# Kernel optimization log

Hardware: AMD Instinct MI355X
Metric: run time of the kernel (lower is better)

The kernel has to match this reference:

```python
import jax, jax.numpy as jnp
import numpy as np

H, KD, VD = 12, 64, 64  # num_heads, k_dim, v_dim
EPS = 1e-12

def _l2norm(x, axis):
    n = jnp.linalg.norm(x, axis=axis, keepdims=True)
    return x / jnp.maximum(n, EPS)

def setup_inputs() -> dict:
    key = jax.random.key(0)
    ks = jax.random.split(key, 6)
    d1, d2 = 768, 768
    return {
        "x1": jax.random.normal(ks[0], (2048, d1), jnp.float32),
        "x2": jax.random.normal(ks[1], (8192, d2), jnp.float32),
        "Wq": jax.random.normal(ks[2], (H * KD, d1), jnp.float32) * 0.03,
        "Wk": jax.random.normal(ks[3], (H * KD, d2), jnp.float32) * 0.03,
        "Wv": jax.random.normal(ks[4], (H * VD, d2), jnp.float32) * 0.03,
        "Wo": jax.random.normal(ks[5], (d1, H * VD), jnp.float32) * 0.03,
        "invt": 20,
    }

def reference(x1, x2, Wq, Wk, Wv, Wo, invt):
    B1 = x1.shape[0]
    B2 = x2.shape[0]
    # Linear (no bias): y = x @ W.T, then split heads
    q = (x1 @ Wq.T).reshape(B1, H, KD)  # [B1,H,KD]
    k = (x2 @ Wk.T).reshape(B2, H, KD)  # [B2,H,KD]
    v = (x2 @ Wv.T).reshape(B2, H, VD)  # [B2,H,VD]
    # per-head L2 normalization over feature dim (cosine attention)
    q = _l2norm(q, axis=-1)
    k = _l2norm(k, axis=-1)
    attn = jnp.einsum("bhd,nhd->hbn", q, k) * jnp.float32(invt)  # [H,B1,B2]
    attn = jax.nn.softmax(attn, axis=-1)
    out = jnp.einsum("hbn,nhd->bhd", attn, v).reshape(B1, H * VD)
    out = out @ Wo.T  # [B1, in_dim1]
    return _l2norm(out, axis=1)
```

## Files before the change

### kernel.cpp

```cpp
#include <hip/hip_runtime.h>
#include <hip/hip_bf16.h>
#include <math.h>

#define B1 2048
#define B2 8192
#define NH 12
#define DH 64
#define DMODEL 768

typedef __attribute__((ext_vector_type(8))) short short8;
typedef __attribute__((ext_vector_type(4))) float floatx4;
typedef __attribute__((ext_vector_type(8))) unsigned short ushort8;
typedef __attribute__((ext_vector_type(4))) unsigned short ushort4v;

static __device__ __forceinline__ unsigned short f2bf(float f) {
  __bf16 b = (__bf16)f;
  return __builtin_bit_cast(unsigned short, b);
}

template <bool L2N, bool F32OUT>
static __device__ __forceinline__ void gemm_tile_f32(
    const float* __restrict__ Ag, const float* __restrict__ Bg,
    void* __restrict__ Cv, int M, int N, int K, int m0, int n0,
    unsigned short* sA, unsigned short* sB) {
  const int tid = threadIdx.x;
  const int wave = tid >> 6;
  const int lane = tid & 63;
  const int wm = wave >> 1;
  const int wn = wave & 1;
  const int n15 = lane & 15;
  const int quad = lane >> 4;
  const int srow = lane >> 2;
  const int cpl = (lane & 3) ^ (srow >> 2);
  const int nstep = K >> 5;

  floatx4 acc[4][4];
#pragma unroll
  for (int i = 0; i < 4; ++i)
#pragma unroll
    for (int j = 0; j < 4; ++j) acc[i][j] = (floatx4){0.f, 0.f, 0.f, 0.f};

  float4 ar[2][2], br[2][2];
#pragma unroll
  for (int jj = 0; jj < 2; ++jj) {
    const int row = (wave * 2 + jj) * 16 + srow;
    const size_t ga = (size_t)(m0 + row) * K + cpl * 8;
    const size_t gb = (size_t)(n0 + row) * K + cpl * 8;
    ar[jj][0] = *(const float4*)&Ag[ga];
    ar[jj][1] = *(const float4*)&Ag[ga + 4];
    br[jj][0] = *(const float4*)&Bg[gb];
    br[jj][1] = *(const float4*)&Bg[gb + 4];
  }
#pragma unroll
  for (int jj = 0; jj < 2; ++jj) {
    const int j = wave * 2 + jj;
    const float4 a0 = ar[jj][0], a1 = ar[jj][1];
    const float4 b0 = br[jj][0], b1 = br[jj][1];
    ushort8 ah = {f2bf(a0.x), f2bf(a0.y), f2bf(a0.z), f2bf(a0.w),
                  f2bf(a1.x), f2bf(a1.y), f2bf(a1.z), f2bf(a1.w)};
    ushort8 bh = {f2bf(b0.x), f2bf(b0.y), f2bf(b0.z), f2bf(b0.w),
                  f2bf(b1.x), f2bf(b1.y), f2bf(b1.z), f2bf(b1.w)};
    *(ushort8*)&sA[j * 512 + lane * 8] = ah;
    *(ushort8*)&sB[j * 512 + lane * 8] = bh;
  }
  if (nstep > 1) {
#pragma unroll
    for (int jj = 0; jj < 2; ++jj) {
      const int row = (wave * 2 + jj) * 16 + srow;
      const size_t ga = (size_t)(m0 + row) * K + 32 + cpl * 8;
      const size_t gb = (size_t)(n0 + row) * K + 32 + cpl * 8;
      ar[jj][0] = *(const float4*)&Ag[ga];
      ar[jj][1] = *(const float4*)&Ag[ga + 4];
      br[jj][0] = *(const float4*)&Bg[gb];
      br[jj][1] = *(const float4*)&Bg[gb + 4];
    }
  }
  __syncthreads();

  for (int k = 0; k < nstep; ++k) {
    const int cb = (k & 1) * 4096;
    if (k + 1 < nstep) {
      const int nb = ((k + 1) & 1) * 4096;
#pragma unroll
      for (int jj = 0; jj < 2; ++jj) {
        const int j = wave * 2 + jj;
        const float4 a0 = ar[jj][0], a1 = ar[jj][1];
        const float4 b0 = br[jj][0], b1 = br[jj][1];
        ushort8 ah = {f2bf(a0.x), f2bf(a0.y), f2bf(a0.z), f2bf(a0.w),
                      f2bf(a1.x), f2bf(a1.y), f2bf(a1.z), f2bf(a1.w)};
        ushort8 bh = {f2bf(b0.x), f2bf(b0.y), f2bf(b0.z), f2bf(b0.w),
                      f2bf(b1.x), f2bf(b1.y), f2bf(b1.z), f2bf(b1.w)};
        *(ushort8*)&sA[nb + j * 512 + lane * 8] = ah;
        *(ushort8*)&sB[nb + j * 512 + lane * 8] = bh;
      }
      if (k + 2 < nstep) {
#pragma unroll
        for (int jj = 0; jj < 2; ++jj) {
          const int row = (wave * 2 + jj) * 16 + srow;
          const size_t ga = (size_t)(m0 + row) * K + (k + 2) * 32 + cpl * 8;
          const size_t gb = (size_t)(n0 + row) * K + (k + 2) * 32 + cpl * 8;
          ar[jj][0] = *(const float4*)&Ag[ga];
          ar[jj][1] = *(const float4*)&Ag[ga + 4];
          br[jj][0] = *(const float4*)&Bg[gb];
          br[jj][1] = *(const float4*)&Bg[gb + 4];
        }
      }
    }

    short8 afh[4];
#pragma unroll
    for (int mt = 0; mt < 4; ++mt) {
      const int row = wm * 64 + mt * 16 + n15;
      afh[mt] = *(const short8*)&sA[cb + row * 32 + ((quad ^ (n15 >> 2)) << 3)];
    }
#pragma unroll
    for (int nt = 0; nt < 4; ++nt) {
      const int row = wn * 64 + nt * 16 + n15;
      const short8 bfh = *(const short8*)&sB[cb + row * 32 + ((quad ^ (n15 >> 2)) << 3)];
#pragma unroll
      for (int mt = 0; mt < 4; ++mt)
        acc[mt][nt] = __builtin_amdgcn_mfma_f32_16x16x32_bf16(afh[mt], bfh, acc[mt][nt], 0, 0, 0);
    }
    __syncthreads();
  }

#pragma unroll
  for (int mt = 0; mt < 4; ++mt) {
    float scalev[4] = {1.f, 1.f, 1.f, 1.f};
    if constexpr (L2N) {
#pragma unroll
      for (int rr = 0; rr < 4; ++rr) {
        float ss = 0.f;
#pragma unroll
        for (int nt = 0; nt < 4; ++nt) ss += acc[mt][nt][rr] * acc[mt][nt][rr];
        ss += __shfl_xor(ss, 1, 64);
        ss += __shfl_xor(ss, 2, 64);
        ss += __shfl_xor(ss, 4, 64);
        ss += __shfl_xor(ss, 8, 64);
        scalev[rr] = 1.0f / fmaxf(sqrtf(ss), 1e-12f);
      }
    }
#pragma unroll
    for (int nt = 0; nt < 4; ++nt) {
#pragma unroll
      for (int rr = 0; rr < 4; ++rr) {
        const int row = m0 + wm * 64 + mt * 16 + quad * 4 + rr;
        const int col = n0 + wn * 64 + nt * 16 + n15;
        const float v = acc[mt][nt][rr] * scalev[rr];
        if constexpr (F32OUT)
          ((float*)Cv)[(size_t)row * N + col] = v;
        else
          ((unsigned short*)Cv)[(size_t)row * N + col] = f2bf(v);
      }
    }
  }
}

__global__ __launch_bounds__(256) void qkv_proj(
    const float* __restrict__ x1, const float* __restrict__ Wq,
    const float* __restrict__ x2, const float* __restrict__ Wk,
    const float* __restrict__ Wv,
    unsigned short* __restrict__ qbf, unsigned short* __restrict__ kbf,
    unsigned short* __restrict__ vtbf) {
  __shared__ __align__(16) unsigned short sA[8192], sB[8192];
  const int bid = blockIdx.x;
  if (bid < 96) {
    const int b = (bid & 7) * 12 + (bid >> 3);
    gemm_tile_f32<true, false>(x1, Wq, qbf, B1, DMODEL, DMODEL,
                               (b / 6) * 128, (b % 6) * 128, sA, sB);
  } else if (bid < 480) {
    const int lb = bid - 96;
    const int b = (lb & 7) * 48 + (lb >> 3);
    gemm_tile_f32<true, false>(x2, Wk, kbf, B2, DMODEL, DMODEL,
                               (b / 6) * 128, (b % 6) * 128, sA, sB);
  } else {
    const int lb = bid - 480;
    const int b = (lb & 7) * 48 + (lb >> 3);
    gemm_tile_f32<false, false>(Wv, x2, vtbf, DMODEL, B2, DMODEL,
                                (b % 6) * 128, (b / 6) * 128, sA, sB);
  }
}

#define KC 128
#define KSPLIT 2
#define NCH (B2 / KSPLIT / KC)
#define PSTR 68

__global__ __launch_bounds__(256, 3) void attn_mfma(
    const unsigned short* __restrict__ qb, const unsigned short* __restrict__ kb,
    const unsigned short* __restrict__ vt, float* __restrict__ aoacc,
    float* __restrict__ lacc, const int* __restrict__ invt_p) {
  __shared__ __align__(16) unsigned short smem[25088];
  unsigned short* Psl = smem + 16384;

  const int bid = blockIdx.x;
  const int swz = (bid & 7) * 96 + (bid >> 3);
  const int zz = swz / 384;
  const int rem = swz - zz * 384;
  const int h = rem >> 5;
  const int q0 = (rem & 31) * 64;

  const float c2 = (float)invt_p[0] * 1.4426950408889634f;
  const int tid = threadIdx.x;
  const int wave = tid >> 6;
  const int lane = tid & 63;
  const int qsub = wave >> 1;
  const int ksub = wave & 1;
  const int n15 = lane & 15;
  const int quad = lane >> 4;
  const int kz0 = zz * (B2 / KSPLIT);

  unsigned short* Ps = &Psl[wave * 32 * PSTR];

  short8 qf[2][2];
#pragma unroll
  for (int qt = 0; qt < 2; ++qt)
#pragma unroll
    for (int ks = 0; ks < 2; ++ks) {
      const int qrow = q0 + qsub * 32 + qt * 16 + n15;
      qf[qt][ks] = *(const short8*)&qb[(size_t)qrow * DMODEL + h * DH + ks * 32 + quad * 8];
    }

  floatx4 oacc[2][4];
#pragma unroll
  for (int qt = 0; qt < 2; ++qt)
#pragma unroll
    for (int nt = 0; nt < 4; ++nt) oacc[qt][nt] = (floatx4){0.f, 0.f, 0.f, 0.f};
  float lsum[2] = {0.f, 0.f};

  const unsigned short* kbp = kb + (size_t)kz0 * DMODEL + h * DH;
  const unsigned short* vbp = vt + (size_t)(h * DH) * B2 + kz0;

  ushort8 kr[4];
#pragma unroll
  for (int i = 0; i < 4; ++i) {
    const int s = i * 256 + tid;
    const int key = s >> 3, cpk = s & 7, chk = cpk ^ (key & 7);
    kr[i] = *(const ushort8*)&kbp[(size_t)key * DMODEL + chk * 8];
  }
#pragma unroll
  for (int i = 0; i < 4; ++i) {
    const int s = i * 256 + tid;
    const int key = s >> 3, cpk = s & 7;
    *(ushort8*)&smem[key * 64 + cpk * 8] = kr[i];
  }
#pragma unroll
  for (int i = 0; i < 4; ++i) {
    const int s = i * 256 + tid;
    const int key = s >> 3, cpk = s & 7, chk = cpk ^ (key & 7);
    kr[i] = *(const ushort8*)&kbp[(size_t)(KC + key) * DMODEL + chk * 8];
  }
  __syncthreads();

  for (int c = 0; c < NCH; ++c) {
    unsigned short* Kb = &smem[(c & 1) * 8192];
    unsigned short* Kn = &smem[((c + 1) & 1) * 8192];
    const unsigned short* vc_ = vbp + c * KC;

    ushort8 vr[8];
#pragma unroll
    for (int ks = 0; ks < 2; ++ks)
#pragma unroll
      for (int nt = 0; nt < 4; ++nt)
        vr[ks * 4 + nt] = *(const ushort8*)&vc_[
            (size_t)(nt * 16 + n15) * B2 + (ksub * 8 + ks * 4 + quad) * 8];

    if (c + 1 < NCH) {
#pragma unroll
      for (int i = 0; i < 4; ++i) {
        const int s = i * 256 + tid;
        const int key = s >> 3, cpk = s & 7;
        *(ushort8*)&Kn[key * 64 + cpk * 8] = kr[i];
      }
      if (c + 2 < NCH) {
        const unsigned short* k2 = kbp + (size_t)(c + 2) * KC * DMODEL;
#pragma unroll
        for (int i = 0; i < 4; ++i) {
          const int s = i * 256 + tid;
          const int key = s >> 3, cpk = s & 7, chk = cpk ^ (key & 7);
          kr[i] = *(const ushort8*)&k2[(size_t)key * DMODEL + chk * 8];
        }
      }
    }

#pragma unroll
    for (int kt = 0; kt < 4; ++kt) {
      floatx4 s0 = {0.f, 0.f, 0.f, 0.f}, s1 = {0.f, 0.f, 0.f, 0.f};
#pragma unroll
      for (int ks = 0; ks < 2; ++ks) {
        const int key = ksub * 64 + kt * 16 + n15;
        const int cp = (ks * 4 + quad) ^ (n15 & 7);
        const short8 kf = *(const short8*)&Kb[key * 64 + cp * 8];
        s0 = __builtin_amdgcn_mfma_f32_16x16x32_bf16(kf, qf[0][ks], s0, 0, 0, 0);
        s1 = __builtin_amdgcn_mfma_f32_16x16x32_bf16(kf, qf[1][ks], s1, 0, 0, 0);
      }
      ushort4v p0, p1;
#pragma unroll
      for (int r = 0; r < 4; ++r) {
        const float e0 = exp2f(fmaf(s0[r], c2, -c2));
        const float e1 = exp2f(fmaf(s1[r], c2, -c2));
        lsum[0] += e0;
        lsum[1] += e1;
        p0[r] = f2bf(e0);
        p1[r] = f2bf(e1);
      }
      *(ushort4v*)&Ps[(0 * 16 + n15) * PSTR + kt * 16 + quad * 4] = p0;
      *(ushort4v*)&Ps[(1 * 16 + n15) * PSTR + kt * 16 + quad * 4] = p1;
    }

#pragma unroll
    for (int ks = 0; ks < 2; ++ks) {
      short8 pa[2];
#pragma unroll
      for (int qt = 0; qt < 2; ++qt)
        pa[qt] = *(const short8*)&Ps[(qt * 16 + n15) * PSTR + ks * 32 + quad * 8];
#pragma unroll
      for (int nt = 0; nt < 4; ++nt) {
        const short8 vf = __builtin_bit_cast(short8, vr[ks * 4 + nt]);
        oacc[0][nt] = __builtin_amdgcn_mfma_f32_16x16x32_bf16(pa[0], vf, oacc[0][nt], 0, 0, 0);
        oacc[1][nt] = __builtin_amdgcn_mfma_f32_16x16x32_bf16(pa[1], vf, oacc[1][nt], 0, 0, 0);
      }
    }

    __syncthreads();
  }

#pragma unroll
  for (int qt = 0; qt < 2; ++qt) {
    float v = lsum[qt];
    v += __shfl_xor(v, 16, 64);
    v += __shfl_xor(v, 32, 64);
    lsum[qt] = v;
  }

  float* aoz = aoacc + (size_t)zz * B1 * DMODEL;
  float* lz = lacc + (size_t)zz * B1 * NH;

  __syncthreads();
  float* Osc = (float*)smem;
  float* lsc = Osc + 4096;
  if (ksub == 1) {
#pragma unroll
    for (int qt = 0; qt < 2; ++qt)
#pragma unroll
      for (int nt = 0; nt < 4; ++nt)
#pragma unroll
        for (int r = 0; r < 4; ++r) {
          const int row = qsub * 32 + qt * 16 + quad * 4 + r;
          Osc[row * 64 + nt * 16 + n15] = oacc[qt][nt][r];
        }
    if (quad == 0) {
      lsc[qsub * 32 + n15] = lsum[0];
      lsc[qsub * 32 + 16 + n15] = lsum[1];
    }
  }
  __syncthreads();
  if (ksub == 0) {
#pragma unroll
    for (int qt = 0; qt < 2; ++qt)
#pragma unroll
      for (int nt = 0; nt < 4; ++nt)
#pragma unroll
        for (int r = 0; r < 4; ++r) {
          const int row = qsub * 32 + qt * 16 + quad * 4 + r;
          const float v = oacc[qt][nt][r] + Osc[row * 64 + nt * 16 + n15];
          aoz[(size_t)(q0 + row) * DMODEL + h * DH + nt * 16 + n15] = v;
        }
    if (quad == 0) {
      lz[(size_t)(q0 + qsub * 32 + n15) * NH + h] = lsum[0] + lsc[qsub * 32 + n15];
      lz[(size_t)(q0 + qsub * 32 + 16 + n15) * NH + h] =
          lsum[1] + lsc[qsub * 32 + 16 + n15];
    }
  }
}

__global__ __launch_bounds__(256) void wo_proj(
    const float* __restrict__ aoacc, const float* __restrict__ lacc,
    const float* __restrict__ Wo, float* __restrict__ woout) {
  __shared__ __align__(16) unsigned short sA[8192], sB[8192];
  const int bid = blockIdx.x;
  const int kz = bid / 96;
  const int lb = bid % 96;
  const int t = (lb & 7) * 12 + (lb >> 3);
  const int m0 = (t / 6) * 128;
  const int n0 = (t % 6) * 128;
  const int kbase = kz * 256;
  const int nstep = 8;
  const int tid = threadIdx.x;
  const int wave = tid >> 6;
  const int lane = tid & 63;
  const int wm = wave >> 1;
  const int wn = wave & 1;
  const int n15 = lane & 15;
  const int quad = lane >> 4;
  const int srow = lane >> 2;
  const int cpl = (lane & 3) ^ (srow >> 2);

  const float* ao1 = aoacc + (size_t)B1 * DMODEL;
  const float* la1 = lacc + (size_t)B1 * NH;

  floatx4 acc[4][4];
#pragma unroll
  for (int i = 0; i < 4; ++i)
#pragma unroll
    for (int j = 0; j < 4; ++j) acc[i][j] = (floatx4){0.f, 0.f, 0.f, 0.f};

  float4 Aa[2][2], Ab[2][2], Bw[2][2];
  float lw[2];

#define WO_LOADSTEP(s)                                                        \
  {                                                                           \
    const int kk = kbase + (s) * 32;                                          \
    _Pragma("unroll") for (int jj = 0; jj < 2; ++jj) {                        \
      const int row = (wave * 2 + jj) * 16 + srow;                            \
      const size_t ga = (size_t)(m0 + row) * DMODEL + kk + cpl * 8;           \
      const size_t gb = (size_t)(n0 + row) * DMODEL + kk + cpl * 8;           \
      Aa[jj][0] = *(const float4*)&aoacc[ga];                                 \
      Aa[jj][1] = *(const float4*)&aoacc[ga + 4];                             \
      Ab[jj][0] = *(const float4*)&ao1[ga];                                   \
      Ab[jj][1] = *(const float4*)&ao1[ga + 4];                               \
      Bw[jj][0] = *(const float4*)&Wo[gb];                                    \
      Bw[jj][1] = *(const float4*)&Wo[gb + 4];                                \
      const int head = (kk + cpl * 8) >> 6;                                   \
      const int li = (m0 + row) * NH + head;                                  \
      lw[jj] = lacc[li] + la1[li];                                            \
    }                                                                         \
  }

#define WO_WRITEBUF(boff)                                                     \
  {                                                                           \
    _Pragma("unroll") for (int jj = 0; jj < 2; ++jj) {                        \
      const int j = wave * 2 + jj;                                            \
      const float inv = 1.0f / lw[jj];                                        \
      const float4 a0 = Aa[jj][0], a1 = Aa[jj][1];                            \
      const float4 b0 = Ab[jj][0], b1 = Ab[jj][1];                            \
      const float4 w0 = Bw[jj][0], w1 = Bw[jj][1];                            \
      ushort8 ah = {f2bf((a0.x + b0.x) * inv), f2bf((a0.y + b0.y) * inv),     \
                    f2bf((a0.z + b0.z) * inv), f2bf((a0.w + b0.w) * inv),     \
                    f2bf((a1.x + b1.x) * inv), f2bf((a1.y + b1.y) * inv),     \
                    f2bf((a1.z + b1.z) * inv), f2bf((a1.w + b1.w) * inv)};    \
      ushort8 bh = {f2bf(w0.x), f2bf(w0.y), f2bf(w0.z), f2bf(w0.w),           \
                    f2bf(w1.x), f2bf(w1.y), f2bf(w1.z), f2bf(w1.w)};          \
      *(ushort8*)&sA[(boff) + j * 512 + lane * 8] = ah;                       \
      *(ushort8*)&sB[(boff) + j * 512 + lane * 8] = bh;                       \
    }                                                                         \
  }

  WO_LOADSTEP(0);
  WO_WRITEBUF(0);
  WO_LOADSTEP(1);
  __syncthreads();

  for (int k = 0; k < nstep; ++k) {
    const int cb = (k & 1) * 4096;
    if (k + 1 < nstep) {
      const int nb = ((k + 1) & 1) * 4096;
      WO_WRITEBUF(nb);
      if (k + 2 < nstep) WO_LOADSTEP(k + 2);
    }

    short8 afh[4];
#pragma unroll
    for (int mt = 0; mt < 4; ++mt) {
      const int row = wm * 64 + mt * 16 + n15;
      afh[mt] = *(const short8*)&sA[cb + row * 32 + ((quad ^ (n15 >> 2)) << 3)];
    }
#pragma unroll
    for (int nt = 0; nt < 4; ++nt) {
      const int row = wn * 64 + nt * 16 + n15;
      const short8 bfh = *(const short8*)&sB[cb + row * 32 + ((quad ^ (n15 >> 2)) << 3)];
#pragma unroll
      for (int mt = 0; mt < 4; ++mt)
        acc[mt][nt] = __builtin_amdgcn_mfma_f32_16x16x32_bf16(afh[mt], bfh, acc[mt][nt], 0, 0, 0);
    }
    __syncthreads();
  }

  float* wslab = woout + (size_t)kz * B1 * DMODEL;
#pragma unroll
  for (int mt = 0; mt < 4; ++mt)
#pragma unroll
    for (int nt = 0; nt < 4; ++nt)
#pragma unroll
      for (int rr = 0; rr < 4; ++rr) {
        const int row = m0 + wm * 64 + mt * 16 + quad * 4 + rr;
        const int col = n0 + wn * 64 + nt * 16 + n15;
        wslab[(size_t)row * DMODEL + col] = acc[mt][nt][rr];
      }
#undef WO_LOADSTEP
#undef WO_WRITEBUF
}

__global__ __launch_bounds__(256) void l2norm_rows768_out(
    const float* __restrict__ x, float* __restrict__ out) {
  const int row = blockIdx.x;
  const float* x0 = &x[(size_t)row * DMODEL];
  const float* x1s = x0 + (size_t)B1 * DMODEL;
  const float* x2s = x0 + 2 * (size_t)B1 * DMODEL;
  float ss = 0.0f;
  float vals[3];
#pragma unroll
  for (int i = 0; i < 3; ++i) {
    const int c = threadIdx.x + i * 256;
    vals[i] = x0[c] + x1s[c] + x2s[c];
    ss += vals[i] * vals[i];
  }
#pragma unroll
  for (int off = 32; off > 0; off >>= 1) ss += __shfl_xor(ss, off, 64);
  __shared__ float ws[4];
  if ((threadIdx.x & 63) == 0) ws[threadIdx.x >> 6] = ss;
  __syncthreads();
  const float tot = ws[0] + ws[1] + ws[2] + ws[3];
  const float sc = 1.0f / fmaxf(sqrtf(tot), 1e-12f);
  float* orow = &out[(size_t)row * DMODEL];
#pragma unroll
  for (int i = 0; i < 3; ++i) orow[threadIdx.x + i * 256] = vals[i] * sc;
}

extern "C" void kernel_launch(void* const* d_in, const int* in_sizes, int n_in,
                              void* d_out, int out_size, void* d_ws,
                              size_t ws_size, hipStream_t stream) {
  const float* x1 = (const float*)d_in[0];
  const float* x2 = (const float*)d_in[1];
  const float* Wq = (const float*)d_in[2];
  const float* Wk = (const float*)d_in[3];
  const float* Wv = (const float*)d_in[4];
  const float* Wo = (const float*)d_in[5];
  const int* invt = (const int*)d_in[6];
  float* outp = (float*)d_out;

  char* ws = (char*)d_ws;
  float* aoacc = (float*)(ws + 0);
  float* woout = (float*)(ws + 12582912);
  unsigned short* vt_bf = (unsigned short*)(ws + 18874368);
  float* lacc = (float*)(ws + 32636928);
  unsigned short* q_bf = (unsigned short*)(ws + 38535168);
  unsigned short* k_bf = (unsigned short*)(ws + 41680896);

  qkv_proj<<<864, 256, 0, stream>>>(x1, Wq, x2, Wk, Wv, q_bf, k_bf, vt_bf);
  attn_mfma<<<768, 256, 0, stream>>>(q_bf, k_bf, vt_bf, aoacc, lacc, invt);
  wo_proj<<<288, 256, 0, stream>>>(aoacc, lacc, Wo, woout);
  l2norm_rows768_out<<<B1, 256, 0, stream>>>(woout, outp);
}
```

Baseline: 270.3 us.

## Split attention key chunk across four waves per query group with 512-thread blocks

Doubles the attention block to 8 waves, each handling 32 keys of the 128-key chunk instead of 64. Per-thread K staging and V register loads are halved, and the final reduction combines four partial output and row-sum slabs through shared memory. The aim is more latency hiding per CU with lower register pressure per wave. The trade-offs are a larger cross-wave reduction and a P stride of 34 that leaves 16-byte LDS reads misaligned.

New measurement: 429.5 us. 58.9% more time.

```diff
diff --git a/kernel.cpp b/kernel.cpp
--- a/kernel.cpp
+++ b/kernel.cpp
@@ -184,9 +184,9 @@
 #define KC 128
 #define KSPLIT 2
 #define NCH (B2 / KSPLIT / KC)
-#define PSTR 68
-
-__global__ __launch_bounds__(256, 3) void attn_mfma(
+#define PSTR 34
+
+__global__ __launch_bounds__(512, 6) void attn_mfma(
     const unsigned short* __restrict__ qb, const unsigned short* __restrict__ kb,
     const unsigned short* __restrict__ vt, float* __restrict__ aoacc,
     float* __restrict__ lacc, const int* __restrict__ invt_p) {
@@ -204,8 +204,8 @@
   const int tid = threadIdx.x;
   const int wave = tid >> 6;
   const int lane = tid & 63;
-  const int qsub = wave >> 1;
-  const int ksub = wave & 1;
+  const int qsub = wave >> 2;
+  const int ksub = wave & 3;
   const int n15 = lane & 15;
   const int quad = lane >> 4;
   const int kz0 = zz * (B2 / KSPLIT);
@@ -231,22 +231,22 @@
   const unsigned short* kbp = kb + (size_t)kz0 * DMODEL + h * DH;
   const unsigned short* vbp = vt + (size_t)(h * DH) * B2 + kz0;
 
-  ushort8 kr[4];
-#pragma unroll
-  for (int i = 0; i < 4; ++i) {
-    const int s = i * 256 + tid;
+  ushort8 kr[2];
+#pragma unroll
+  for (int i = 0; i < 2; ++i) {
+    const int s = i * 512 + tid;
     const int key = s >> 3, cpk = s & 7, chk = cpk ^ (key & 7);
     kr[i] = *(const ushort8*)&kbp[(size_t)key * DMODEL + chk * 8];
   }
 #pragma unroll
-  for (int i = 0; i < 4; ++i) {
-    const int s = i * 256 + tid;
+  for (int i = 0; i < 2; ++i) {
+    const int s = i * 512 + tid;
     const int key = s >> 3, cpk = s & 7;
     *(ushort8*)&smem[key * 64 + cpk * 8] = kr[i];
   }
 #pragma unroll
-  for (int i = 0; i < 4; ++i) {
-    const int s = i * 256 + tid;
+  for (int i = 0; i < 2; ++i) {
+    const int s = i * 512 + tid;
     const int key = s >> 3, cpk = s & 7, chk = cpk ^ (key & 7);
     kr[i] = *(const ushort8*)&kbp[(size_t)(KC + key) * DMODEL + chk * 8];
   }
@@ -257,26 +257,24 @@
     unsigned short* Kn = &smem[((c + 1) & 1) * 8192];
     const unsigned short* vc_ = vbp + c * KC;
 
-    ushort8 vr[8];
-#pragma unroll
-    for (int ks = 0; ks < 2; ++ks)
-#pragma unroll
-      for (int nt = 0; nt < 4; ++nt)
-        vr[ks * 4 + nt] = *(const ushort8*)&vc_[
-            (size_t)(nt * 16 + n15) * B2 + (ksub * 8 + ks * 4 + quad) * 8];
+    ushort8 vr[4];
+#pragma unroll
+    for (int nt = 0; nt < 4; ++nt)
+      vr[nt] = *(const ushort8*)&vc_[
+          (size_t)(nt * 16 + n15) * B2 + (ksub * 4 + quad) * 8];
 
     if (c + 1 < NCH) {
 #pragma unroll
-      for (int i = 0; i < 4; ++i) {
-        const int s = i * 256 + tid;
+      for (int i = 0; i < 2; ++i) {
+        const int s = i * 512 + tid;
         const int key = s >> 3, cpk = s & 7;
         *(ushort8*)&Kn[key * 64 + cpk * 8] = kr[i];
       }
       if (c + 2 < NCH) {
         const unsigned short* k2 = kbp + (size_t)(c + 2) * KC * DMODEL;
 #pragma unroll
-        for (int i = 0; i < 4; ++i) {
-          const int s = i * 256 + tid;
+        for (int i = 0; i < 2; ++i) {
+          const int s = i * 512 + tid;
           const int key = s >> 3, cpk = s & 7, chk = cpk ^ (key & 7);
           kr[i] = *(const ushort8*)&k2[(size_t)key * DMODEL + chk * 8];
         }
@@ -284,13 +282,13 @@
     }
 
 #pragma unroll
-    for (int kt = 0; kt < 4; ++kt) {
+    for (int kt = 0; kt < 2; ++kt) {
       floatx4 s0 = {0.f, 0.f, 0.f, 0.f}, s1 = {0.f, 0.f, 0.f, 0.f};
 #pragma unroll
       for (int ks = 0; ks < 2; ++ks) {
-        const int key = ksub * 64 + kt * 16 + n15;
+        const int keyrow = ksub * 32 + kt * 16 + n15;
         const int cp = (ks * 4 + quad) ^ (n15 & 7);
-        const short8 kf = *(const short8*)&Kb[key * 64 + cp * 8];
+        const short8 kf = *(const short8*)&Kb[keyrow * 64 + cp * 8];
         s0 = __builtin_amdgcn_mfma_f32_16x16x32_bf16(kf, qf[0][ks], s0, 0, 0, 0);
         s1 = __builtin_amdgcn_mfma_f32_16x16x32_bf16(kf, qf[1][ks], s1, 0, 0, 0);
       }
@@ -308,15 +306,14 @@
       *(ushort4v*)&Ps[(1 * 16 + n15) * PSTR + kt * 16 + quad * 4] = p1;
     }
 
-#pragma unroll
-    for (int ks = 0; ks < 2; ++ks) {
+    {
       short8 pa[2];
 #pragma unroll
       for (int qt = 0; qt < 2; ++qt)
-        pa[qt] = *(const short8*)&Ps[(qt * 16 + n15) * PSTR + ks * 32 + quad * 8];
+        pa[qt] = *(const short8*)&Ps[(qt * 16 + n15) * PSTR + quad * 8];
 #pragma unroll
       for (int nt = 0; nt < 4; ++nt) {
-        const short8 vf = __builtin_bit_cast(short8, vr[ks * 4 + nt]);
+        const short8 vf = __builtin_bit_cast(short8, vr[nt]);
         oacc[0][nt] = __builtin_amdgcn_mfma_f32_16x16x32_bf16(pa[0], vf, oacc[0][nt], 0, 0, 0);
         oacc[1][nt] = __builtin_amdgcn_mfma_f32_16x16x32_bf16(pa[1], vf, oacc[1][nt], 0, 0, 0);
       }
@@ -338,8 +335,9 @@
 
   __syncthreads();
   float* Osc = (float*)smem;
-  float* lsc = Osc + 4096;
-  if (ksub == 1) {
+  float* lsc = Osc + 3 * 4096;
+  if (ksub != 0) {
+    float* slab = Osc + (ksub - 1) * 4096;
 #pragma unroll
     for (int qt = 0; qt < 2; ++qt)
 #pragma unroll
@@ -347,11 +345,11 @@
 #pragma unroll
         for (int r = 0; r < 4; ++r) {
           const int row = qsub * 32 + qt * 16 + quad * 4 + r;
-          Osc[row * 64 + nt * 16 + n15] = oacc[qt][nt][r];
+          slab[row * 64 + nt * 16 + n15] = oacc[qt][nt][r];
         }
     if (quad == 0) {
-      lsc[qsub * 32 + n15] = lsum[0];
-      lsc[qsub * 32 + 16 + n15] = lsum[1];
+      lsc[(ksub - 1) * 64 + qsub * 32 + n15] = lsum[0];
+      lsc[(ksub - 1) * 64 + qsub * 32 + 16 + n15] = lsum[1];
     }
   }
   __syncthreads();
@@ -363,13 +361,18 @@
 #pragma unroll
         for (int r = 0; r < 4; ++r) {
           const int row = qsub * 32 + qt * 16 + quad * 4 + r;
-          const float v = oacc[qt][nt][r] + Osc[row * 64 + nt * 16 + n15];
-          aoz[(size_t)(q0 + row) * DMODEL + h * DH + nt * 16 + n15] = v;
+          const int cc = nt * 16 + n15;
+          const float v = oacc[qt][nt][r] + Osc[row * 64 + cc] +
+                          Osc[4096 + row * 64 + cc] + Osc[8192 + row * 64 + cc];
+          aoz[(size_t)(q0 + row) * DMODEL + h * DH + cc] = v;
         }
     if (quad == 0) {
-      lz[(size_t)(q0 + qsub * 32 + n15) * NH + h] = lsum[0] + lsc[qsub * 32 + n15];
-      lz[(size_t)(q0 + qsub * 32 + 16 + n15) * NH + h] =
-          lsum[1] + lsc[qsub * 32 + 16 + n15];
+      const int b0 = qsub * 32 + n15;
+      const int b1 = qsub * 32 + 16 + n15;
+      lz[(size_t)(q0 + b0) * NH + h] =
+          lsum[0] + lsc[b0] + lsc[64 + b0] + lsc[128 + b0];
+      lz[(size_t)(q0 + b1) * NH + h] =
+          lsum[1] + lsc[b1] + lsc[64 + b1] + lsc[128 + b1];
     }
   }
 }
@@ -538,7 +541,7 @@
   unsigned short* k_bf = (unsigned short*)(ws + 41680896);
 
   qkv_proj<<<864, 256, 0, stream>>>(x1, Wq, x2, Wk, Wv, q_bf, k_bf, vt_bf);
-  attn_mfma<<<768, 256, 0, stream>>>(q_bf, k_bf, vt_bf, aoacc, lacc, invt);
+  attn_mfma<<<768, 512, 0, stream>>>(q_bf, k_bf, vt_bf, aoacc, lacc, invt);
   wo_proj<<<288, 256, 0, stream>>>(aoacc, lacc, Wo, woout);
   l2norm_rows768_out<<<B1, 256, 0, stream>>>(woout, outp);
 }
```
